# Kernel tuning notes

Measured on AMD Instinct MI355X. Metric: run time of the kernel, lower is better.

## Reference

```python
import jax, jax.numpy as jnp
import numpy as np

H, D, EF, NT, ET = 4, 32, 32, 4, 8
N, E = 100000, 1600000
NEG_SLOPE = 0.2


def setup_inputs() -> dict:
    key = jax.random.key(0)
    ks = jax.random.split(key, 11)
    return {
        "feat": jax.random.normal(ks[0], (N, H * D), jnp.float32),
        "fc": jax.random.normal(ks[1], (NT, H, D), jnp.float32) * 0.1,
        "edge_emb": jax.random.normal(ks[2], (ET, EF), jnp.float32),
        "W_e": jax.random.normal(ks[3], (H * EF, EF), jnp.float32) * 0.1,
        "attn_l": jax.random.normal(ks[4], (1, H, D), jnp.float32) * 0.1,
        "attn_r": jax.random.normal(ks[5], (1, H, D), jnp.float32) * 0.1,
        "attn_e": jax.random.normal(ks[6], (1, H, EF), jnp.float32) * 0.1,
        "node_types": jax.random.randint(ks[7], (N,), 0, NT, jnp.int32),
        "e_feat": jax.random.randint(ks[8], (E,), 0, ET, jnp.int32),
        "src": jax.random.randint(ks[9], (E,), 0, N, jnp.int32),
        "dst": jax.random.randint(ks[10], (E,), 0, N, jnp.int32),
    }


def reference(feat, fc, edge_emb, W_e, attn_l, attn_r, attn_e, node_types, e_feat, src, dst):
    n = feat.shape[0]
    h = feat.reshape(n, H, D)                      # [N,H,D] (h_src == h_dst)
    fs = h * fc[node_types]                        # per-node-type scaling, feat_src == feat_dst

    # edge-type embedding path: Embedding -> Linear(edge_feats, H*edge_feats) -> attn_e score
    emb = (edge_emb @ W_e.T).reshape(ET, H, EF)    # [ET,H,EF]
    ee = (emb * attn_e).sum(-1)[e_feat]            # [E,H]

    el = (fs * attn_l).sum(-1)                     # [N,H]
    er = (fs * attn_r).sum(-1)                     # [N,H]
    e = jax.nn.leaky_relu(el[src] + er[dst] + ee, NEG_SLOPE)  # [E,H]

    # edge_softmax: segment softmax over destination node
    m = jax.ops.segment_max(e, dst, num_segments=n)           # [N,H]
    ex = jnp.exp(e - m[dst])
    s = jax.ops.segment_sum(ex, dst, num_segments=n)          # [N,H]
    a = ex / s[dst]                                            # [E,H]

    # u_mul_e + sum aggregation
    msg = fs[src] * a[:, :, None]                              # [E,H,D]
    rst = jax.ops.segment_sum(msg, dst, num_segments=n)       # [N,H,D]

    rst = rst + h                                              # residual (Identity, in==out feats)
    return rst, a[:, :, None]
```

## Files before the change

### kernel.cpp

```cpp
#include <hip/hip_runtime.h>
#include <stdint.h>

namespace {
constexpr int kH = 4, kD = 32, kEF = 32, kNT = 4, kET = 8;
constexpr int kHD = kH * kD;
constexpr float kNegSlope = 0.2f;
constexpr int kBN = 128;
constexpr int kNB = (100000 + kBN - 1) / kBN;
constexpr int kHB = 512;
constexpr int kIB = 2048;
constexpr int kCap = 4096;
constexpr int kXP = 20;

using f32x2 = __attribute__((ext_vector_type(2))) float;
using f32x4 = __attribute__((ext_vector_type(4))) float;

__device__ __forceinline__ float lrelu(float x) { return x > 0.f ? x : kNegSlope * x; }

__global__ void __launch_bounds__(256) k_init(
    const float* __restrict__ feat, const float* __restrict__ fc,
    const float* __restrict__ edge_emb, const float* __restrict__ W_e,
    const float* __restrict__ attn_l, const float* __restrict__ attn_r,
    const float* __restrict__ attn_e, const int* __restrict__ node_types,
    const int* __restrict__ dst, const int* __restrict__ src,
    const int* __restrict__ e_feat, int* __restrict__ cursor,
    int* __restrict__ tmp, float* __restrict__ el, float* __restrict__ ernv,
    uint8_t* __restrict__ fs, float* __restrict__ ee_tab, int N, int E) {
  __shared__ int h[kNB], r[kNB];
  int t = threadIdx.x;
  if (blockIdx.x < kHB) {
    for (int i = t; i < kNB; i += 256) h[i] = 0;
    __syncthreads();
    int per = (E + kHB - 1) / kHB;
    int e0 = blockIdx.x * per;
    int e1 = min(e0 + per, E);
    for (int i = e0 + t; i < e1; i += 256) atomicAdd(&h[dst[i] >> 7], 1);
    __syncthreads();
    for (int i = t; i < kNB; i += 256) {
      int c = h[i];
      r[i] = i * kCap + (c ? atomicAdd(&cursor[i], c) : 0);
    }
    __syncthreads();
    for (int i = e0 + t; i < e1; i += 256) {
      int d = dst[i];
      int b = d >> 7;
      int pos = atomicAdd(&r[b], 1);
      tmp[pos] = src[i] | (e_feat[i] << 17) | ((d & 127) << 20);
    }
  }
  if (blockIdx.x == 0 && t < kET * kH) {
    int et = t / kH, hh = t % kH;
    float acc = 0.f;
    for (int f = 0; f < kEF; ++f) {
      const float* wrow = W_e + (hh * kEF + f) * kEF;
      const float* erow = edge_emb + et * kEF;
      float emb = 0.f;
      for (int k = 0; k < kEF; ++k) emb += erow[k] * wrow[k];
      acc += emb * attn_e[hh * kEF + f];
    }
    ee_tab[et * kH + hh] = acc;
  }
  int lane = t & 31;
  float4 al = *(const float4*)(attn_l + lane * 4);
  float4 ar = *(const float4*)(attn_r + lane * 4);
  int ngTot = (N + 7) >> 3;
  for (int ng = blockIdx.x; ng < ngTot; ng += gridDim.x) {
    int node = (ng << 3) + (t >> 5);
    if (node >= N) continue;
    int nt = node_types[node];
    float4 f4 = *(const float4*)(feat + ((size_t)node << 7) + lane * 4);
    float4 c4 = *(const float4*)(fc + nt * kHD + lane * 4);
    float fx = f4.x * c4.x, fy = f4.y * c4.y, fz = f4.z * c4.z, fw = f4.w * c4.w;
    int w = __builtin_amdgcn_cvt_pk_fp8_f32(fx, fy, 0, false);
    w = __builtin_amdgcn_cvt_pk_fp8_f32(fz, fw, w, true);
    *(int*)(fs + ((size_t)node << 7) + lane * 4) = w;
    float pl = fx * al.x + fy * al.y + fz * al.z + fw * al.w;
    float pr = fx * ar.x + fy * ar.y + fz * ar.z + fw * ar.w;
#pragma unroll
    for (int off = 1; off < 8; off <<= 1) {
      pl += __shfl_xor(pl, off);
      pr += __shfl_xor(pr, off);
    }
    if ((lane & 7) == 0) {
      int hh = lane >> 3;
      el[node * kH + hh] = pl;
      ernv[(node << 3) + hh] = pr;
    }
  }
}

__global__ void __launch_bounds__(256) k_build(const int* __restrict__ cursor,
                                               const int* __restrict__ tmp,
                                               int* __restrict__ ptr,
                                               int* __restrict__ csr, int N, int E) {
  __shared__ int fh[128], fb[128], sc[128];
  __shared__ int red[256];
  int b = blockIdx.x, t = threadIdx.x;
  int acc = 0;
  for (int i = t; i < b; i += 256) acc += cursor[i];
  red[t] = acc;
  __syncthreads();
  for (int off = 128; off > 0; off >>= 1) {
    if (t < off) red[t] += red[t + off];
    __syncthreads();
  }
  int s0 = red[0];
  int cnt = min(cursor[b], kCap);
  const int* slab = tmp + (size_t)b * kCap;
  if (t < 128) fh[t] = 0;
  __syncthreads();
  for (int j = t; j < cnt; j += 256) atomicAdd(&fh[slab[j] >> 20], 1);
  __syncthreads();
  if (t < 128) sc[t] = fh[t];
  __syncthreads();
  for (int off = 1; off < 128; off <<= 1) {
    int v = 0;
    if (t < 128 && t >= off) v = sc[t - off];
    __syncthreads();
    if (t < 128) sc[t] += v;
    __syncthreads();
  }
  if (t < 128) {
    fb[t] = sc[t] - fh[t];
    int d = (b << 7) + t;
    if (d < N) ptr[d] = s0 + fb[t];
    fh[t] = 0;
  }
  if (b == gridDim.x - 1 && t == 0) ptr[N] = E;
  __syncthreads();
  for (int j = t; j < cnt; j += 256) {
    int v = slab[j];
    int dl = v >> 20;
    int r = atomicAdd(&fh[dl], 1);
    csr[s0 + fb[dl] + r] = v & 0xFFFFF;
  }
}

__global__ void __launch_bounds__(256) k_fused(
    const uint8_t* __restrict__ fs, const float* __restrict__ feat,
    const float* __restrict__ el, float* __restrict__ ernv,
    const float* __restrict__ ee_tab, const int* __restrict__ ptr,
    const int* __restrict__ csr, float* __restrict__ rst, int N) {
  __shared__ float ee_sh[kET * kH];
  __shared__ __align__(16) float xp[4][64 * kXP];
  if (threadIdx.x < kET * kH) ee_sh[threadIdx.x] = ee_tab[threadIdx.x];
  __syncthreads();
  int lane = threadIdx.x & 63;
  int wid = threadIdx.x >> 6;
  int node = blockIdx.x * 4 + wid;
  if (node >= N) return;
  int start = ptr[node], end = ptr[node + 1];

  int g = lane >> 3;
  int q = lane & 7;
  int head = q >> 1;
  int qoff = q << 4;
  float er_h = ernv[(node << 3) + head];
  f32x2 f2 = *(const f32x2*)(feat + ((size_t)node << 7) + lane * 2);

  float sm = 0.f;
  f32x2 acc[8];
#pragma unroll
  for (int k = 0; k < 8; ++k) acc[k] = (f32x2){0.f, 0.f};

  int j = start + g;
  int pk0 = csr[(j < end) ? j : 0];
  int pk1 = csr[(j + 8 < end) ? j + 8 : 0];
  int s0 = pk0 & 0x1FFFF;
  float elv0 = el[(s0 << 2) + head];
  int4 w0 = *(const int4*)(fs + ((size_t)s0 << 7) + qoff);
  float ee0 = ee_sh[((pk0 >> 17) << 2) + head];
  int s1 = pk1 & 0x1FFFF;
  float elv1 = el[(s1 << 2) + head];
  int4 w1 = *(const int4*)(fs + ((size_t)s1 << 7) + qoff);
  float ee1 = ee_sh[((pk1 >> 17) << 2) + head];
  int pk2 = csr[(j + 16 < end) ? j + 16 : 0];

  while (j < end) {
    int s2 = pk2 & 0x1FFFF;
    float elv2 = el[(s2 << 2) + head];
    int4 w2 = *(const int4*)(fs + ((size_t)s2 << 7) + qoff);
    float ee2 = ee_sh[((pk2 >> 17) << 2) + head];
    int pk3 = csr[(j + 24 < end) ? j + 24 : 0];
    float ex = __expf(lrelu(elv0 + er_h + ee0));
    sm += ex;
    f32x2 ex2 = {ex, ex};
#pragma unroll
    for (int c = 0; c < 4; ++c) {
      int wc = c == 0 ? w0.x : c == 1 ? w0.y : c == 2 ? w0.z : w0.w;
      acc[2 * c + 0] += ex2 * __builtin_amdgcn_cvt_pk_f32_fp8(wc, false);
      acc[2 * c + 1] += ex2 * __builtin_amdgcn_cvt_pk_f32_fp8(wc, true);
    }
    elv0 = elv1; w0 = w1; ee0 = ee1;
    elv1 = elv2; w1 = w2; ee1 = ee2;
    pk2 = pk3;
    j += 8;
  }

  sm += __shfl_xor(sm, 8);
  sm += __shfl_xor(sm, 16);
  sm += __shfl_xor(sm, 32);
  float rinv = sm > 0.f ? 1.f / sm : 0.f;

  float* row = &xp[wid][lane * kXP];
#pragma unroll
  for (int c = 0; c < 4; ++c) {
    float4 v4 = {acc[2 * c].x, acc[2 * c].y, acc[2 * c + 1].x, acc[2 * c + 1].y};
    *(float4*)(row + c * 4) = v4;
  }
  asm volatile("s_waitcnt lgkmcnt(0)" ::: "memory");
  __builtin_amdgcn_sched_barrier(0);
  int qsrc = lane >> 3;
  int coff = (lane & 7) * 2;
  const float* base = &xp[wid][qsrc * kXP + coff];
  f32x2 v = {0.f, 0.f};
#pragma unroll
  for (int gg = 0; gg < 8; ++gg) v += *(const f32x2*)(base + gg * 8 * kXP);

  float rs = __shfl(rinv, (lane >> 4) << 1);
  float rb = __shfl(rinv, lane << 1);
  f32x2 o = v * rs + f2;
  __builtin_nontemporal_store(o, (f32x2*)(rst + ((size_t)node << 7) + lane * 2));
  if (lane < kH) ernv[(node << 3) + 4 + lane] = rb;
}

__global__ void __launch_bounds__(256) k_post(
    const int* __restrict__ src, const int* __restrict__ dst,
    const int* __restrict__ e_feat, const float* __restrict__ el,
    const float* __restrict__ ernv, const float* __restrict__ ee_tab,
    float* __restrict__ out_a, int E) {
  int i = blockIdx.x * blockDim.x + threadIdx.x;
  if (i >= E) return;
  int s = src[i], d = dst[i], et = e_feat[i];
  float4 elv = *(const float4*)(el + s * kH);
  float4 erv = *(const float4*)(ernv + ((size_t)d << 3));
  float4 rv = *(const float4*)(ernv + ((size_t)d << 3) + 4);
  float4 ee = *(const float4*)(ee_tab + et * kH);
  f32x4 a;
  a.x = __expf(lrelu(elv.x + erv.x + ee.x)) * rv.x;
  a.y = __expf(lrelu(elv.y + erv.y + ee.y)) * rv.y;
  a.z = __expf(lrelu(elv.z + erv.z + ee.z)) * rv.z;
  a.w = __expf(lrelu(elv.w + erv.w + ee.w)) * rv.w;
  __builtin_nontemporal_store(a, (f32x4*)(out_a + (size_t)i * kH));
}

}

extern "C" void kernel_launch(void* const* d_in, const int* in_sizes, int n_in,
                              void* d_out, int out_size, void* d_ws, size_t ws_size,
                              hipStream_t stream) {
  const float* feat = (const float*)d_in[0];
  const float* fc = (const float*)d_in[1];
  const float* edge_emb = (const float*)d_in[2];
  const float* W_e = (const float*)d_in[3];
  const float* attn_l = (const float*)d_in[4];
  const float* attn_r = (const float*)d_in[5];
  const float* attn_e = (const float*)d_in[6];
  const int* node_types = (const int*)d_in[7];
  const int* e_feat = (const int*)d_in[8];
  const int* src = (const int*)d_in[9];
  const int* dst = (const int*)d_in[10];
  int N = in_sizes[7];
  int E = in_sizes[8];

  char* ws = (char*)d_ws;
  size_t off = 0;
  auto alloc = [&](size_t bytes) -> void* {
    void* p = ws + off;
    off = (off + bytes + 255) & ~(size_t)255;
    return p;
  };
  float* ee_tab = (float*)alloc((size_t)kET * kH * sizeof(float));
  float* el = (float*)alloc((size_t)N * kH * sizeof(float));
  float* ernv = (float*)alloc((size_t)N * 2 * kH * sizeof(float));
  uint8_t* fs = (uint8_t*)alloc((size_t)N * kHD * sizeof(uint8_t));
  int* cursor = (int*)alloc((size_t)kNB * sizeof(int));
  int* ptr = (int*)alloc((size_t)(N + 1) * sizeof(int));
  int* tmp = (int*)alloc((size_t)kNB * kCap * sizeof(int));
  int* csr = (int*)alloc((size_t)E * sizeof(int));

  hipMemsetAsync(cursor, 0, (size_t)kNB * sizeof(int), stream);
  k_init<<<kIB, 256, 0, stream>>>(feat, fc, edge_emb, W_e, attn_l, attn_r,
                                  attn_e, node_types, dst, src, e_feat,
                                  cursor, tmp, el, ernv, fs, ee_tab, N, E);
  k_build<<<kNB, 256, 0, stream>>>(cursor, tmp, ptr, csr, N, E);

  float* rst = (float*)d_out;
  float* out_a = (float*)d_out + (size_t)N * kHD;
  k_fused<<<(N + 3) / 4, 256, 0, stream>>>(fs, feat, el, ernv, ee_tab, ptr, csr,
                                           rst, N);
  k_post<<<(E + 255) / 256, 256, 0, stream>>>(src, dst, e_feat, el, ernv, ee_tab,
                                              out_a, E);
}
```

Baseline: 287.9 us.

## Fuse attention-weight output into aggregation kernel by carrying edge ids through CSR

The edge id is now stored alongside the packed source/type word in the bucketed temp and CSR arrays. The aggregation kernel buffers each edge's exp values in LDS and writes the normalized attention directly, scattered to the original edge position, so the separate per-edge post kernel and its rereads of src/dst/e_feat/el/er are removed. High-degree nodes recompute the exp values in a second pass. The init kernel also switches from a grid-stride loop to one node per 32 lanes with a larger grid. The trade-off is doubled CSR and temp traffic, plus scattered 16-byte stores to out_a instead of coalesced ones.

```diff
diff --git a/kernel.cpp b/kernel.cpp
--- a/kernel.cpp
+++ b/kernel.cpp
@@ -8,7 +8,6 @@
 constexpr int kBN = 128;
 constexpr int kNB = (100000 + kBN - 1) / kBN;
 constexpr int kHB = 512;
-constexpr int kIB = 2048;
 constexpr int kCap = 4096;
 constexpr int kXP = 20;
 
@@ -24,7 +23,7 @@
     const float* __restrict__ attn_e, const int* __restrict__ node_types,
     const int* __restrict__ dst, const int* __restrict__ src,
     const int* __restrict__ e_feat, int* __restrict__ cursor,
-    int* __restrict__ tmp, float* __restrict__ el, float* __restrict__ ernv,
+    int2* __restrict__ tmp, float* __restrict__ el, float* __restrict__ er,
     uint8_t* __restrict__ fs, float* __restrict__ ee_tab, int N, int E) {
   __shared__ int h[kNB], r[kNB];
   int t = threadIdx.x;
@@ -45,7 +44,8 @@
       int d = dst[i];
       int b = d >> 7;
       int pos = atomicAdd(&r[b], 1);
-      tmp[pos] = src[i] | (e_feat[i] << 17) | ((d & 127) << 20);
+      int2 v2 = {src[i] | (e_feat[i] << 17) | ((d & 127) << 20), i};
+      tmp[pos] = v2;
     }
   }
   if (blockIdx.x == 0 && t < kET * kH) {
@@ -60,39 +60,37 @@
     }
     ee_tab[et * kH + hh] = acc;
   }
+  int gid = blockIdx.x * blockDim.x + t;
+  int node = gid >> 5;
   int lane = t & 31;
+  if (node >= N) return;
+  int nt = node_types[node];
+  float4 f4 = *(const float4*)(feat + ((size_t)node << 7) + lane * 4);
+  float4 c4 = *(const float4*)(fc + nt * kHD + lane * 4);
   float4 al = *(const float4*)(attn_l + lane * 4);
   float4 ar = *(const float4*)(attn_r + lane * 4);
-  int ngTot = (N + 7) >> 3;
-  for (int ng = blockIdx.x; ng < ngTot; ng += gridDim.x) {
-    int node = (ng << 3) + (t >> 5);
-    if (node >= N) continue;
-    int nt = node_types[node];
-    float4 f4 = *(const float4*)(feat + ((size_t)node << 7) + lane * 4);
-    float4 c4 = *(const float4*)(fc + nt * kHD + lane * 4);
-    float fx = f4.x * c4.x, fy = f4.y * c4.y, fz = f4.z * c4.z, fw = f4.w * c4.w;
-    int w = __builtin_amdgcn_cvt_pk_fp8_f32(fx, fy, 0, false);
-    w = __builtin_amdgcn_cvt_pk_fp8_f32(fz, fw, w, true);
-    *(int*)(fs + ((size_t)node << 7) + lane * 4) = w;
-    float pl = fx * al.x + fy * al.y + fz * al.z + fw * al.w;
-    float pr = fx * ar.x + fy * ar.y + fz * ar.z + fw * ar.w;
-#pragma unroll
-    for (int off = 1; off < 8; off <<= 1) {
-      pl += __shfl_xor(pl, off);
-      pr += __shfl_xor(pr, off);
-    }
-    if ((lane & 7) == 0) {
-      int hh = lane >> 3;
-      el[node * kH + hh] = pl;
-      ernv[(node << 3) + hh] = pr;
-    }
+  float fx = f4.x * c4.x, fy = f4.y * c4.y, fz = f4.z * c4.z, fw = f4.w * c4.w;
+  int w = __builtin_amdgcn_cvt_pk_fp8_f32(fx, fy, 0, false);
+  w = __builtin_amdgcn_cvt_pk_fp8_f32(fz, fw, w, true);
+  *(int*)(fs + ((size_t)node << 7) + lane * 4) = w;
+  float pl = fx * al.x + fy * al.y + fz * al.z + fw * al.w;
+  float pr = fx * ar.x + fy * ar.y + fz * ar.z + fw * ar.w;
+#pragma unroll
+  for (int off = 1; off < 8; off <<= 1) {
+    pl += __shfl_xor(pl, off);
+    pr += __shfl_xor(pr, off);
+  }
+  if ((lane & 7) == 0) {
+    int hh = lane >> 3;
+    el[node * kH + hh] = pl;
+    er[node * kH + hh] = pr;
   }
 }
 
 __global__ void __launch_bounds__(256) k_build(const int* __restrict__ cursor,
-                                               const int* __restrict__ tmp,
+                                               const int2* __restrict__ tmp,
                                                int* __restrict__ ptr,
-                                               int* __restrict__ csr, int N, int E) {
+                                               int2* __restrict__ csr2, int N, int E) {
   __shared__ int fh[128], fb[128], sc[128];
   __shared__ int red[256];
   int b = blockIdx.x, t = threadIdx.x;
@@ -106,10 +104,10 @@
   }
   int s0 = red[0];
   int cnt = min(cursor[b], kCap);
-  const int* slab = tmp + (size_t)b * kCap;
+  const int2* slab = tmp + (size_t)b * kCap;
   if (t < 128) fh[t] = 0;
   __syncthreads();
-  for (int j = t; j < cnt; j += 256) atomicAdd(&fh[slab[j] >> 20], 1);
+  for (int j = t; j < cnt; j += 256) atomicAdd(&fh[slab[j].x >> 20], 1);
   __syncthreads();
   if (t < 128) sc[t] = fh[t];
   __syncthreads();
@@ -129,18 +127,20 @@
   if (b == gridDim.x - 1 && t == 0) ptr[N] = E;
   __syncthreads();
   for (int j = t; j < cnt; j += 256) {
-    int v = slab[j];
-    int dl = v >> 20;
+    int2 v = slab[j];
+    int dl = v.x >> 20;
     int r = atomicAdd(&fh[dl], 1);
-    csr[s0 + fb[dl] + r] = v & 0xFFFFF;
+    int2 o = {v.x & 0xFFFFF, v.y};
+    csr2[s0 + fb[dl] + r] = o;
   }
 }
 
 __global__ void __launch_bounds__(256) k_fused(
     const uint8_t* __restrict__ fs, const float* __restrict__ feat,
-    const float* __restrict__ el, float* __restrict__ ernv,
+    const float* __restrict__ el, const float* __restrict__ er,
     const float* __restrict__ ee_tab, const int* __restrict__ ptr,
-    const int* __restrict__ csr, float* __restrict__ rst, int N) {
+    const int2* __restrict__ csr2, float* __restrict__ rst,
+    float* __restrict__ out_a, int N) {
   __shared__ float ee_sh[kET * kH];
   __shared__ __align__(16) float xp[4][64 * kXP];
   if (threadIdx.x < kET * kH) ee_sh[threadIdx.x] = ee_tab[threadIdx.x];
@@ -150,13 +150,18 @@
   int node = blockIdx.x * 4 + wid;
   if (node >= N) return;
   int start = ptr[node], end = ptr[node + 1];
+  int deg = end - start;
+  bool big = deg > 64;
 
   int g = lane >> 3;
   int q = lane & 7;
   int head = q >> 1;
   int qoff = q << 4;
-  float er_h = ernv[(node << 3) + head];
+  float er_h = er[(node << 2) + head];
   f32x2 f2 = *(const f32x2*)(feat + ((size_t)node << 7) + lane * 2);
+
+  float* exb = &xp[wid][0];
+  int* eidb = (int*)&xp[wid][1024];
 
   float sm = 0.f;
   f32x2 acc[8];
@@ -164,26 +169,31 @@
   for (int k = 0; k < 8; ++k) acc[k] = (f32x2){0.f, 0.f};
 
   int j = start + g;
-  int pk0 = csr[(j < end) ? j : 0];
-  int pk1 = csr[(j + 8 < end) ? j + 8 : 0];
-  int s0 = pk0 & 0x1FFFF;
+  int2 pk0 = csr2[(j < end) ? j : 0];
+  int2 pk1 = csr2[(j + 8 < end) ? j + 8 : 0];
+  int s0 = pk0.x & 0x1FFFF;
   float elv0 = el[(s0 << 2) + head];
   int4 w0 = *(const int4*)(fs + ((size_t)s0 << 7) + qoff);
-  float ee0 = ee_sh[((pk0 >> 17) << 2) + head];
-  int s1 = pk1 & 0x1FFFF;
+  float ee0 = ee_sh[((pk0.x >> 17) << 2) + head];
+  int s1 = pk1.x & 0x1FFFF;
   float elv1 = el[(s1 << 2) + head];
   int4 w1 = *(const int4*)(fs + ((size_t)s1 << 7) + qoff);
-  float ee1 = ee_sh[((pk1 >> 17) << 2) + head];
-  int pk2 = csr[(j + 16 < end) ? j + 16 : 0];
-
+  float ee1 = ee_sh[((pk1.x >> 17) << 2) + head];
+  int2 pk2 = csr2[(j + 16 < end) ? j + 16 : 0];
+
+  int le = g;
   while (j < end) {
-    int s2 = pk2 & 0x1FFFF;
+    int s2 = pk2.x & 0x1FFFF;
     float elv2 = el[(s2 << 2) + head];
     int4 w2 = *(const int4*)(fs + ((size_t)s2 << 7) + qoff);
-    float ee2 = ee_sh[((pk2 >> 17) << 2) + head];
-    int pk3 = csr[(j + 24 < end) ? j + 24 : 0];
+    float ee2 = ee_sh[((pk2.x >> 17) << 2) + head];
+    int2 pk3 = csr2[(j + 24 < end) ? j + 24 : 0];
     float ex = __expf(lrelu(elv0 + er_h + ee0));
     sm += ex;
+    if (!big) {
+      if ((q & 1) == 0) exb[(le << 2) + head] = ex;
+      if (q == 7) eidb[le] = pk0.y;
+    }
     f32x2 ex2 = {ex, ex};
 #pragma unroll
     for (int c = 0; c < 4; ++c) {
@@ -191,16 +201,46 @@
       acc[2 * c + 0] += ex2 * __builtin_amdgcn_cvt_pk_f32_fp8(wc, false);
       acc[2 * c + 1] += ex2 * __builtin_amdgcn_cvt_pk_f32_fp8(wc, true);
     }
-    elv0 = elv1; w0 = w1; ee0 = ee1;
-    elv1 = elv2; w1 = w2; ee1 = ee2;
+    elv0 = elv1; w0 = w1; ee0 = ee1; pk0 = pk1;
+    elv1 = elv2; w1 = w2; ee1 = ee2; pk1 = pk2;
     pk2 = pk3;
     j += 8;
+    le += 8;
   }
 
   sm += __shfl_xor(sm, 8);
   sm += __shfl_xor(sm, 16);
   sm += __shfl_xor(sm, 32);
   float rinv = sm > 0.f ? 1.f / sm : 0.f;
+  float rv0 = __shfl(rinv, 0), rv1 = __shfl(rinv, 2);
+  float rv2 = __shfl(rinv, 4), rv3 = __shfl(rinv, 6);
+
+  if (!big) {
+    asm volatile("s_waitcnt lgkmcnt(0)" ::: "memory");
+    __builtin_amdgcn_sched_barrier(0);
+    if (lane < deg) {
+      float4 e4 = *(const float4*)(exb + (lane << 2));
+      int eid = eidb[lane];
+      f32x4 a = {e4.x * rv0, e4.y * rv1, e4.z * rv2, e4.w * rv3};
+      __builtin_nontemporal_store(a, (f32x4*)(out_a + ((size_t)eid << 2)));
+    }
+    __builtin_amdgcn_sched_barrier(0);
+  } else {
+    for (int jj = start + g; jj < end; jj += 8) {
+      int2 pk = csr2[jj];
+      int ss = pk.x & 0x1FFFF;
+      float e_h = lrelu(el[(ss << 2) + head] + er_h +
+                        ee_sh[((pk.x >> 17) << 2) + head]);
+      float ex = __expf(e_h);
+      float exA = __shfl_down(ex, 2);
+      float exB = __shfl_down(ex, 4);
+      float exC = __shfl_down(ex, 6);
+      if (q == 0) {
+        f32x4 a = {ex * rv0, exA * rv1, exB * rv2, exC * rv3};
+        __builtin_nontemporal_store(a, (f32x4*)(out_a + ((size_t)pk.y << 2)));
+      }
+    }
+  }
 
   float* row = &xp[wid][lane * kXP];
 #pragma unroll
@@ -218,30 +258,8 @@
   for (int gg = 0; gg < 8; ++gg) v += *(const f32x2*)(base + gg * 8 * kXP);
 
   float rs = __shfl(rinv, (lane >> 4) << 1);
-  float rb = __shfl(rinv, lane << 1);
   f32x2 o = v * rs + f2;
   __builtin_nontemporal_store(o, (f32x2*)(rst + ((size_t)node << 7) + lane * 2));
-  if (lane < kH) ernv[(node << 3) + 4 + lane] = rb;
-}
-
-__global__ void __launch_bounds__(256) k_post(
-    const int* __restrict__ src, const int* __restrict__ dst,
-    const int* __restrict__ e_feat, const float* __restrict__ el,
-    const float* __restrict__ ernv, const float* __restrict__ ee_tab,
-    float* __restrict__ out_a, int E) {
-  int i = blockIdx.x * blockDim.x + threadIdx.x;
-  if (i >= E) return;
-  int s = src[i], d = dst[i], et = e_feat[i];
-  float4 elv = *(const float4*)(el + s * kH);
-  float4 erv = *(const float4*)(ernv + ((size_t)d << 3));
-  float4 rv = *(const float4*)(ernv + ((size_t)d << 3) + 4);
-  float4 ee = *(const float4*)(ee_tab + et * kH);
-  f32x4 a;
-  a.x = __expf(lrelu(elv.x + erv.x + ee.x)) * rv.x;
-  a.y = __expf(lrelu(elv.y + erv.y + ee.y)) * rv.y;
-  a.z = __expf(lrelu(elv.z + erv.z + ee.z)) * rv.z;
-  a.w = __expf(lrelu(elv.w + erv.w + ee.w)) * rv.w;
-  __builtin_nontemporal_store(a, (f32x4*)(out_a + (size_t)i * kH));
 }
 
 }
@@ -272,23 +290,21 @@
   };
   float* ee_tab = (float*)alloc((size_t)kET * kH * sizeof(float));
   float* el = (float*)alloc((size_t)N * kH * sizeof(float));
-  float* ernv = (float*)alloc((size_t)N * 2 * kH * sizeof(float));
+  float* er = (float*)alloc((size_t)N * kH * sizeof(float));
   uint8_t* fs = (uint8_t*)alloc((size_t)N * kHD * sizeof(uint8_t));
   int* cursor = (int*)alloc((size_t)kNB * sizeof(int));
   int* ptr = (int*)alloc((size_t)(N + 1) * sizeof(int));
-  int* tmp = (int*)alloc((size_t)kNB * kCap * sizeof(int));
-  int* csr = (int*)alloc((size_t)E * sizeof(int));
+  int2* tmp = (int2*)alloc((size_t)kNB * kCap * sizeof(int2));
+  int2* csr2 = (int2*)alloc((size_t)E * sizeof(int2));
 
   hipMemsetAsync(cursor, 0, (size_t)kNB * sizeof(int), stream);
-  k_init<<<kIB, 256, 0, stream>>>(feat, fc, edge_emb, W_e, attn_l, attn_r,
-                                  attn_e, node_types, dst, src, e_feat,
-                                  cursor, tmp, el, ernv, fs, ee_tab, N, E);
-  k_build<<<kNB, 256, 0, stream>>>(cursor, tmp, ptr, csr, N, E);
+  k_init<<<(N + 7) / 8, 256, 0, stream>>>(feat, fc, edge_emb, W_e, attn_l, attn_r,
+                                          attn_e, node_types, dst, src, e_feat,
+                                          cursor, tmp, el, er, fs, ee_tab, N, E);
+  k_build<<<kNB, 256, 0, stream>>>(cursor, tmp, ptr, csr2, N, E);
 
   float* rst = (float*)d_out;
   float* out_a = (float*)d_out + (size_t)N * kHD;
-  k_fused<<<(N + 3) / 4, 256, 0, stream>>>(fs, feat, el, ernv, ee_tab, ptr, csr,
-                                           rst, N);
-  k_post<<<(E + 255) / 256, 256, 0, stream>>>(src, dst, e_feat, el, ernv, ee_tab,
-                                              out_a, E);
-}
+  k_fused<<<(N + 3) / 4, 256, 0, stream>>>(fs, feat, el, er, ee_tab, ptr, csr2,
+                                           rst, out_a, N);
+}
```

After: 278.6 us. 1.03x faster.
